# Performance work log

Hardware: AMD Instinct MI355X
Metric: run time of the kernel (lower is better)

## Reference

```python
import jax, jax.numpy as jnp
import numpy as np

B, S = 1, 2048
HID, NH, NKV, HD = 2048, 16, 4, 128
NREP = NH // NKV  # 4
WIN = 1024
ROPE_THETA = 10000.0


def rotate_half(t):
    t1, t2 = jnp.split(t, 2, axis=-1)
    return jnp.concatenate([-t2, t1], axis=-1)


def setup_inputs() -> dict:
    key = jax.random.key(0)
    ks = jax.random.split(key, 5)
    x = jax.random.normal(ks[0], (B, S, HID), dtype=jnp.float32)
    # causal sliding-window additive mask: 0 where attended, -1e9 elsewhere
    i = jnp.arange(S)
    allowed = (i[None, :] <= i[:, None]) & (i[:, None] - i[None, :] < WIN)
    attention_mask = jnp.where(allowed, 0.0, -1e9).astype(jnp.float32)[None, None]  # [1,1,S,S]
    wq = jax.random.normal(ks[1], (NH * HD, HID), dtype=jnp.float32) * 0.02
    wk = jax.random.normal(ks[2], (NKV * HD, HID), dtype=jnp.float32) * 0.02
    wv = jax.random.normal(ks[3], (NKV * HD, HID), dtype=jnp.float32) * 0.02
    wo = jax.random.normal(ks[4], (HID, NH * HD), dtype=jnp.float32) * 0.02
    return {"x": x, "attention_mask": attention_mask, "wq": wq, "wk": wk, "wv": wv, "wo": wo}


def reference(x, attention_mask, wq, wk, wv, wo):
    b, s, _ = x.shape
    q = (x @ wq.T).reshape(b, s, NH, HD)
    k = (x @ wk.T).reshape(b, s, NKV, HD)
    v = (x @ wv.T).reshape(b, s, NKV, HD)
    # rotary embeddings (HF-style rotate_half)
    inv_freq = 1.0 / (ROPE_THETA ** (jnp.arange(0, HD, 2, dtype=jnp.float32) / HD))
    freqs = jnp.arange(s, dtype=jnp.float32)[:, None] * inv_freq[None, :]  # [s, HD/2]
    emb = jnp.concatenate([freqs, freqs], axis=-1)  # [s, HD]
    cos = jnp.cos(emb)[None, :, None, :]
    sin = jnp.sin(emb)[None, :, None, :]
    q = q * cos + rotate_half(q) * sin
    k = k * cos + rotate_half(k) * sin
    # GQA: repeat kv heads
    k = jnp.repeat(k, NREP, axis=2)  # [b, s, NH, HD]
    v = jnp.repeat(v, NREP, axis=2)
    scores = jnp.einsum('bqhd,bkhd->bhqk', q, k) / jnp.sqrt(jnp.float32(HD)) + attention_mask
    probs = jax.nn.softmax(scores.astype(jnp.float32), axis=-1).astype(q.dtype)
    out = jnp.einsum('bhqk,bkhd->bqhd', probs, v).reshape(b, s, NH * HD)
    return out @ wo.T
```

## Files before the change

### kernel.cpp

```cpp
#include <hip/hip_runtime.h>


#define AS1 __attribute__((address_space(1)))
#define AS3 __attribute__((address_space(3)))

typedef short v8s __attribute__((ext_vector_type(8)));
typedef short v4s __attribute__((ext_vector_type(4)));
typedef float v4f __attribute__((ext_vector_type(4)));

__device__ __forceinline__ void gload16(const void* g, void* l) {
  __builtin_amdgcn_global_load_lds((AS1 void*)g, (AS3 void*)l, 16, 0, 0);
}

__device__ __forceinline__ short f2bf(float f) {
  union { float f; unsigned u; } v; v.f = f;
  unsigned r = (v.u + 0x7FFFu + ((v.u >> 16) & 1u)) >> 16;
  return (short)r;
}
__device__ __forceinline__ float bf2f(short h) {
  union { unsigned u; float f; } v; v.u = ((unsigned)(unsigned short)h) << 16;
  return v.f;
}
__device__ __forceinline__ bool sniff_bf16(const unsigned* mask) {
  return mask[1] == 0xCE6ECE6Eu;
}

template <bool BF> struct Raw8;
template <> struct Raw8<true>  { v8s v; };
template <> struct Raw8<false> { float4 a, b; };

template <bool BF> __device__ __forceinline__ Raw8<BF> ldraw(const void* p, size_t e);
template <> __device__ __forceinline__ Raw8<true> ldraw<true>(const void* p, size_t e) {
  Raw8<true> r; r.v = *(const v8s*)((const short*)p + e); return r;
}
template <> __device__ __forceinline__ Raw8<false> ldraw<false>(const void* p, size_t e) {
  Raw8<false> r; const float* f = (const float*)p + e;
  r.a = *(const float4*)f; r.b = *(const float4*)(f + 4); return r;
}
template <bool BF> __device__ __forceinline__ v8s cvt8(const Raw8<BF>& r);
template <> __device__ __forceinline__ v8s cvt8<true>(const Raw8<true>& r) { return r.v; }
template <> __device__ __forceinline__ v8s cvt8<false>(const Raw8<false>& r) {
  v8s o;
  o[0] = f2bf(r.a.x); o[1] = f2bf(r.a.y); o[2] = f2bf(r.a.z); o[3] = f2bf(r.a.w);
  o[4] = f2bf(r.b.x); o[5] = f2bf(r.b.y); o[6] = f2bf(r.b.z); o[7] = f2bf(r.b.w);
  return o;
}

__global__ __launch_bounds__(256) void convert_kernel(
    const void* __restrict__ X, const void* __restrict__ WQ,
    const void* __restrict__ WK, const void* __restrict__ WV,
    const void* __restrict__ WO, const unsigned* __restrict__ mask,
    short* __restrict__ Xbf, short* __restrict__ Wqkvbf, short* __restrict__ WObf)
{
  const bool bf = sniff_bf16(mask);
  size_t e = ((size_t)blockIdx.x * 256 + threadIdx.x) * 8;
  const void* src; short* dst; size_t off, doff;
  if (e < 4194304)       { src = X;  dst = Xbf;  off = e; doff = e; }
  else if (e < 10485760) {
    size_t wv = e - 4194304; dst = Wqkvbf; doff = wv;
    if (wv < 4194304)      { src = WQ; off = wv; }
    else if (wv < 5242880) { src = WK; off = wv - 4194304; }
    else                   { src = WV; off = wv - 5242880; }
  }
  else                   { src = WO; dst = WObf; off = e - 10485760; doff = off; }
  v8s v = bf ? ldraw<true>(src, off).v : cvt8<false>(ldraw<false>(src, off));
  *(v8s*)&dst[doff] = v;
}

__device__ __forceinline__ void gemm_dma_loop(
    const short* __restrict__ A, const short* __restrict__ Bt,
    int m0, int brow0, short* lA, short* lB, v4f acc[2][4])
{
  const int tid = threadIdx.x;
  const int w = tid >> 6, lane = tid & 63;
  const int quad = lane >> 4, r = lane & 15;
  const int wm = (w >> 1) * 32, wn = (w & 1) * 64;
  const int rlo = lane >> 2, c8 = (lane & 3) * 8;

  size_t ga[2]; short* la[2];
#pragma unroll
  for (int j = 0; j < 2; ++j) {
    int cA = w * 2 + j;
    int p = cA >> 2, local = cA & 3;
    ga[j] = (size_t)(m0 + local * 16 + rlo) * 2048 + p * 32 + c8;
    la[j] = lA + cA * 512;
  }
  size_t gb[4]; short* lb[4];
#pragma unroll
  for (int j = 0; j < 4; ++j) {
    int cB = w * 4 + j;
    int p = cB >> 3, local = cB & 7;
    gb[j] = (size_t)(brow0 + local * 16 + rlo) * 2048 + p * 32 + c8;
    lb[j] = lB + cB * 512;
  }

  for (int k0 = 0; k0 < 2048; k0 += 64) {
    if (k0) __syncthreads();
#pragma unroll
    for (int j = 0; j < 2; ++j) gload16(A + ga[j] + k0, la[j]);
#pragma unroll
    for (int j = 0; j < 4; ++j) gload16(Bt + gb[j] + k0, lb[j]);
    __syncthreads();
#pragma unroll
    for (int ks = 0; ks < 2; ++ks) {
      v8s a[2], b[4];
#pragma unroll
      for (int mt = 0; mt < 2; ++mt)
        a[mt] = *(const v8s*)&lA[ks * 2048 + (wm + mt * 16 + r) * 32 + quad * 8];
#pragma unroll
      for (int nt = 0; nt < 4; ++nt)
        b[nt] = *(const v8s*)&lB[ks * 4096 + (wn + nt * 16 + r) * 32 + quad * 8];
#pragma unroll
      for (int mt = 0; mt < 2; ++mt)
#pragma unroll
        for (int nt = 0; nt < 4; ++nt)
          acc[mt][nt] = __builtin_amdgcn_mfma_f32_16x16x32_bf16(a[mt], b[nt], acc[mt][nt], 0, 0, 0);
    }
  }
}

__device__ __forceinline__ void qkv_epilogue(
    v4f acc[2][4], int m0, int n0, short* Qo, short* Ko, short* VTo)
{
  const int tid = threadIdx.x;
  const int w = tid >> 6, lane = tid & 63;
  const int quad = lane >> 4, r = lane & 15;
  const int wm = (w >> 1) * 32, wn = (w & 1) * 64;
  const int rowb = m0 + wm + quad * 4;

  if (n0 < 2048) {
#pragma unroll
    for (int mt = 0; mt < 2; ++mt)
#pragma unroll
      for (int nt = 0; nt < 4; ++nt) {
        int row = rowb + mt * 16;
        int col = n0 + wn + nt * 16 + r;
#pragma unroll
        for (int i = 0; i < 4; ++i)
          Qo[(size_t)(row + i) * 2048 + col] = f2bf(acc[mt][nt][i]);
      }
  } else if (n0 < 2560) {
#pragma unroll
    for (int mt = 0; mt < 2; ++mt)
#pragma unroll
      for (int nt = 0; nt < 4; ++nt) {
        int row = rowb + mt * 16;
        int col = n0 + wn + nt * 16 + r - 2048;
#pragma unroll
        for (int i = 0; i < 4; ++i)
          Ko[(size_t)(row + i) * 512 + col] = f2bf(acc[mt][nt][i]);
      }
  } else {
#pragma unroll
    for (int mt = 0; mt < 2; ++mt)
#pragma unroll
      for (int nt = 0; nt < 4; ++nt) {
        int row = rowb + mt * 16;
        int vcol = n0 + wn + nt * 16 + r - 2560;
        v4s pk;
#pragma unroll
        for (int i = 0; i < 4; ++i) pk[i] = f2bf(acc[mt][nt][i]);
        *(v4s*)&VTo[(size_t)vcol * 2048 + row] = pk;
      }
  }
}

__global__ __launch_bounds__(256, 3) void gemm_qkv_dma(
    const short* __restrict__ Xbf, const short* __restrict__ Wqkvbf,
    short* __restrict__ Qo, short* __restrict__ Ko, short* __restrict__ VTo)
{
  __shared__ __align__(16) short lA[64 * 64];
  __shared__ __align__(16) short lB[128 * 64];
  const int m0 = blockIdx.x * 64;
  const int n0 = blockIdx.y * 128;
  v4f acc[2][4];
#pragma unroll
  for (int i = 0; i < 2; ++i)
#pragma unroll
    for (int j = 0; j < 4; ++j) acc[i][j] = v4f{0.f, 0.f, 0.f, 0.f};
  gemm_dma_loop(Xbf, Wqkvbf, m0, n0, lA, lB, acc);
  qkv_epilogue(acc, m0, n0, Qo, Ko, VTo);
}

__global__ __launch_bounds__(256, 3) void gemm_out_dma(
    const short* __restrict__ A, const short* __restrict__ WObf,
    const unsigned* __restrict__ mask, void* __restrict__ Out)
{
  __shared__ __align__(16) short lA[64 * 64];
  __shared__ __align__(16) short lB[128 * 64];
  const int m0 = blockIdx.x * 64;
  const int n0 = blockIdx.y * 128;
  v4f acc[2][4];
#pragma unroll
  for (int i = 0; i < 2; ++i)
#pragma unroll
    for (int j = 0; j < 4; ++j) acc[i][j] = v4f{0.f, 0.f, 0.f, 0.f};
  gemm_dma_loop(A, WObf, m0, n0, lA, lB, acc);

  const bool bf = sniff_bf16(mask);
  const int tid = threadIdx.x;
  const int w = tid >> 6, lane = tid & 63;
  const int quad = lane >> 4, r = lane & 15;
  const int wm = (w >> 1) * 32, wn = (w & 1) * 64;
  const int rowb = m0 + wm + quad * 4;
#pragma unroll
  for (int mt = 0; mt < 2; ++mt)
#pragma unroll
    for (int nt = 0; nt < 4; ++nt) {
      int row = rowb + mt * 16;
      int col = n0 + wn + nt * 16 + r;
#pragma unroll
      for (int i = 0; i < 4; ++i) {
        size_t idx = (size_t)(row + i) * 2048 + col;
        if (bf) ((short*)Out)[idx] = f2bf(acc[mt][nt][i]);
        else    ((float*)Out)[idx] = acc[mt][nt][i];
      }
    }
}

template <bool BFA, bool BFB>
__device__ __forceinline__ void gemm64x128_loop(
    const void* __restrict__ A, const void* __restrict__ Bt,
    int m0, int brow0, short* lA, short* lB, v4f acc[2][4])
{
  const int tid = threadIdx.x;
  const int w = tid >> 6, lane = tid & 63;
  const int quad = lane >> 4, r = lane & 15;
  const int wm = (w >> 1) * 32, wn = (w & 1) * 64;

  int uoffA[2]; size_t ea[2];
#pragma unroll
  for (int j = 0; j < 2; ++j) {
    int u = tid + 256 * j;
    int row = u >> 3, c = (u & 7) * 8;
    uoffA[j] = (c & 32) * 64 + row * 32 + (c & 31);
    ea[j] = (size_t)(m0 + row) * 2048 + c;
  }
  int uoffB[4]; size_t eb[4];
#pragma unroll
  for (int j = 0; j < 4; ++j) {
    int u = tid + 256 * j;
    int row = u >> 3, c = (u & 7) * 8;
    uoffB[j] = (c & 32) * 128 + row * 32 + (c & 31);
    eb[j] = (size_t)(brow0 + row) * 2048 + c;
  }

  for (int k0 = 0; k0 < 2048; k0 += 64) {
    Raw8<BFA> ta[2]; Raw8<BFB> tb[4];
#pragma unroll
    for (int j = 0; j < 2; ++j) ta[j] = ldraw<BFA>(A, ea[j] + k0);
#pragma unroll
    for (int j = 0; j < 4; ++j) tb[j] = ldraw<BFB>(Bt, eb[j] + k0);
    if (k0) __syncthreads();
#pragma unroll
    for (int j = 0; j < 2; ++j) *(v8s*)&lA[uoffA[j]] = cvt8<BFA>(ta[j]);
#pragma unroll
    for (int j = 0; j < 4; ++j) *(v8s*)&lB[uoffB[j]] = cvt8<BFB>(tb[j]);
    __syncthreads();
#pragma unroll
    for (int ks = 0; ks < 2; ++ks) {
      v8s a[2], b[4];
#pragma unroll
      for (int mt = 0; mt < 2; ++mt)
        a[mt] = *(const v8s*)&lA[ks * 2048 + (wm + mt * 16 + r) * 32 + quad * 8];
#pragma unroll
      for (int nt = 0; nt < 4; ++nt)
        b[nt] = *(const v8s*)&lB[ks * 4096 + (wn + nt * 16 + r) * 32 + quad * 8];
#pragma unroll
      for (int mt = 0; mt < 2; ++mt)
#pragma unroll
        for (int nt = 0; nt < 4; ++nt)
          acc[mt][nt] = __builtin_amdgcn_mfma_f32_16x16x32_bf16(a[mt], b[nt], acc[mt][nt], 0, 0, 0);
    }
  }
}

__global__ __launch_bounds__(256, 3) void gemm_qkv_fb(
    const void* __restrict__ X, const void* __restrict__ WQ,
    const void* __restrict__ WK, const void* __restrict__ WV,
    const unsigned* __restrict__ mask,
    short* __restrict__ Qo, short* __restrict__ Ko, short* __restrict__ VTo)
{
  __shared__ __align__(16) short lA[64 * 64];
  __shared__ __align__(16) short lB[128 * 64];
  const int m0 = blockIdx.x * 64;
  const int n0 = blockIdx.y * 128;
  const void* Bt; int brow0;
  if (n0 < 2048)      { Bt = WQ; brow0 = n0; }
  else if (n0 < 2560) { Bt = WK; brow0 = n0 - 2048; }
  else                { Bt = WV; brow0 = n0 - 2560; }

  v4f acc[2][4];
#pragma unroll
  for (int i = 0; i < 2; ++i)
#pragma unroll
    for (int j = 0; j < 4; ++j) acc[i][j] = v4f{0.f, 0.f, 0.f, 0.f};

  if (sniff_bf16(mask)) gemm64x128_loop<true, true>(X, Bt, m0, brow0, lA, lB, acc);
  else                  gemm64x128_loop<false, false>(X, Bt, m0, brow0, lA, lB, acc);
  qkv_epilogue(acc, m0, n0, Qo, Ko, VTo);
}

__global__ __launch_bounds__(256, 3) void gemm_out_fb(
    const short* __restrict__ A, const void* __restrict__ WO,
    const unsigned* __restrict__ mask, void* __restrict__ Out)
{
  __shared__ __align__(16) short lA[64 * 64];
  __shared__ __align__(16) short lB[128 * 64];
  const bool bf = sniff_bf16(mask);
  const int m0 = blockIdx.x * 64;
  const int n0 = blockIdx.y * 128;

  v4f acc[2][4];
#pragma unroll
  for (int i = 0; i < 2; ++i)
#pragma unroll
    for (int j = 0; j < 4; ++j) acc[i][j] = v4f{0.f, 0.f, 0.f, 0.f};

  if (bf) gemm64x128_loop<true, true>(A, WO, m0, n0, lA, lB, acc);
  else    gemm64x128_loop<true, false>(A, WO, m0, n0, lA, lB, acc);

  const int tid = threadIdx.x;
  const int w = tid >> 6, lane = tid & 63;
  const int quad = lane >> 4, r = lane & 15;
  const int wm = (w >> 1) * 32, wn = (w & 1) * 64;
  const int rowb = m0 + wm + quad * 4;
#pragma unroll
  for (int mt = 0; mt < 2; ++mt)
#pragma unroll
    for (int nt = 0; nt < 4; ++nt) {
      int row = rowb + mt * 16;
      int col = n0 + wn + nt * 16 + r;
#pragma unroll
      for (int i = 0; i < 4; ++i) {
        size_t idx = (size_t)(row + i) * 2048 + col;
        if (bf) ((short*)Out)[idx] = f2bf(acc[mt][nt][i]);
        else    ((float*)Out)[idx] = acc[mt][nt][i];
      }
    }
}

__global__ __launch_bounds__(256) void rope_kernel(short* __restrict__ Q, short* __restrict__ K)
{
  const int t = blockIdx.x * 256 + threadIdx.x;
  const float L2T = 13.287712379549449f / 64.0f;
  int s, d; short* p; float scale;
  if (t < 2097152) {
    s = t >> 10; int rem = t & 1023; int h = rem >> 6; d = rem & 63;
    p = Q + (size_t)s * 2048 + h * 128 + d;
    scale = 0.08838834764831845f;
  } else {
    int u = t - 2097152;
    s = u >> 8; int rem = u & 255; int h = rem >> 6; d = rem & 63;
    p = K + (size_t)s * 512 + h * 128 + d;
    scale = 1.0f;
  }
  float inv = exp2f(-(float)d * L2T);
  float ang = (float)s * inv;
  float cs = cosf(ang), sn = sinf(ang);
  float x1 = bf2f(p[0]), x2 = bf2f(p[64]);
  p[0]  = f2bf((x1 * cs - x2 * sn) * scale);
  p[64] = f2bf((x2 * cs + x1 * sn) * scale);
}

__global__ __launch_bounds__(256, 1) void attn_kernel(
    const short* __restrict__ Q, const short* __restrict__ Kb,
    const short* __restrict__ VT, short* __restrict__ Ao)
{
  __shared__ __align__(16) short lK[64 * 128];
  __shared__ __align__(16) short lV[128 * 64];
  __shared__ __align__(16) short lP[4][16 * 72];

  const int bx = blockIdx.x;
  const int h = bx >> 5, qb = bx & 31;
  const int hk = h >> 2;
  const int q0 = qb * 64;
  const int tid = threadIdx.x, w = tid >> 6, lane = tid & 63;
  const int quad = lane >> 4, r = lane & 15;
  const int wq0 = q0 + w * 16;
  short* lPw = lP[w];

  v8s qa[4];
#pragma unroll
  for (int ks = 0; ks < 4; ++ks)
    qa[ks] = *(const v8s*)(Q + (size_t)(wq0 + r) * 2048 + h * 128 + ks * 32 + quad * 8);

  v4f Oa[8];
#pragma unroll
  for (int dt = 0; dt < 8; ++dt) Oa[dt] = v4f{0.f, 0.f, 0.f, 0.f};
  const float NEG = -3.0e38f;
  float m_i[4], l_i[4];
#pragma unroll
  for (int i = 0; i < 4; ++i) { m_i[i] = NEG; l_i[i] = 0.f; }

  const int t0 = (q0 >= 1024) ? ((q0 - 1023) >> 6) : 0;
  const int t1 = qb;

  for (int t = t0; t <= t1; ++t) {
    const int key0 = t << 6;
    v8s tK[4], tV[4];
#pragma unroll
    for (int u = 0; u < 4; ++u) {
      int lin = (w * 4 + u) * 64 + lane;
      int krow = lin >> 4, kcc = lin & 15;
      tK[u] = *(const v8s*)(Kb + (size_t)(key0 + krow) * 512 + hk * 128 + ((kcc ^ krow) & 15) * 8);
      int vrow = lin >> 3, vcc = lin & 7;
      tV[u] = *(const v8s*)(VT + (size_t)(hk * 128 + vrow) * 2048 + key0 + ((vcc ^ vrow) & 7) * 8);
    }
    if (t > t0) __syncthreads();
#pragma unroll
    for (int u = 0; u < 4; ++u) {
      int lin = (w * 4 + u) * 64 + lane;
      *(v8s*)&lK[lin * 8] = tK[u];
      *(v8s*)&lV[lin * 8] = tV[u];
    }
    __syncthreads();

    v4f s4[4];
#pragma unroll
    for (int nt = 0; nt < 4; ++nt) s4[nt] = v4f{0.f, 0.f, 0.f, 0.f};
#pragma unroll
    for (int ks = 0; ks < 4; ++ks)
#pragma unroll
      for (int nt = 0; nt < 4; ++nt) {
        v8s bk = *(const v8s*)&lK[(nt * 16 + r) * 128 + (((ks * 4 + quad) ^ r) & 15) * 8];
        s4[nt] = __builtin_amdgcn_mfma_f32_16x16x32_bf16(qa[ks], bk, s4[nt], 0, 0, 0);
      }

    float rowmax[4] = {NEG, NEG, NEG, NEG};
#pragma unroll
    for (int nt = 0; nt < 4; ++nt) {
      int key = key0 + nt * 16 + r;
#pragma unroll
      for (int i = 0; i < 4; ++i) {
        int q = wq0 + quad * 4 + i;
        bool ok = (key <= q) && (q - key < 1024);
        if (ok) rowmax[i] = fmaxf(rowmax[i], s4[nt][i]);
      }
    }
#pragma unroll
    for (int i = 0; i < 4; ++i)
#pragma unroll
      for (int off = 1; off < 16; off <<= 1)
        rowmax[i] = fmaxf(rowmax[i], __shfl_xor(rowmax[i], off, 64));
    float alpha[4], rsum[4] = {0.f, 0.f, 0.f, 0.f};
#pragma unroll
    for (int i = 0; i < 4; ++i) {
      float mn = fmaxf(m_i[i], rowmax[i]);
      alpha[i] = __expf(m_i[i] - mn);
      m_i[i] = mn;
    }
#pragma unroll
    for (int nt = 0; nt < 4; ++nt) {
      int key = key0 + nt * 16 + r;
#pragma unroll
      for (int i = 0; i < 4; ++i) {
        int q = wq0 + quad * 4 + i;
        bool ok = (key <= q) && (q - key < 1024);
        float p = ok ? __expf(s4[nt][i] - m_i[i]) : 0.0f;
        rsum[i] += p;
        lPw[(quad * 4 + i) * 72 + nt * 16 + r] = f2bf(p);
      }
    }
#pragma unroll
    for (int i = 0; i < 4; ++i) {
#pragma unroll
      for (int off = 1; off < 16; off <<= 1)
        rsum[i] += __shfl_xor(rsum[i], off, 64);
      l_i[i] = l_i[i] * alpha[i] + rsum[i];
    }
#pragma unroll
    for (int dt = 0; dt < 8; ++dt)
#pragma unroll
      for (int i = 0; i < 4; ++i) Oa[dt][i] *= alpha[i];

#pragma unroll
    for (int ks2 = 0; ks2 < 2; ++ks2) {
      v8s ap = *(const v8s*)&lPw[r * 72 + ks2 * 32 + quad * 8];
#pragma unroll
      for (int dt = 0; dt < 8; ++dt) {
        v8s bv = *(const v8s*)&lV[(dt * 16 + r) * 64 + (((ks2 * 4 + quad) ^ r) & 7) * 8];
        Oa[dt] = __builtin_amdgcn_mfma_f32_16x16x32_bf16(ap, bv, Oa[dt], 0, 0, 0);
      }
    }
  }

  float invl[4];
#pragma unroll
  for (int i = 0; i < 4; ++i) invl[i] = (l_i[i] > 0.f) ? 1.0f / l_i[i] : 0.f;
#pragma unroll
  for (int dt = 0; dt < 8; ++dt)
#pragma unroll
    for (int i = 0; i < 4; ++i) {
      int q = wq0 + quad * 4 + i;
      Ao[(size_t)q * 2048 + h * 128 + dt * 16 + r] = f2bf(Oa[dt][i] * invl[i]);
    }
}

extern "C" void kernel_launch(void* const* d_in, const int* in_sizes, int n_in,
                              void* d_out, int out_size, void* d_ws, size_t ws_size,
                              hipStream_t stream) {
  const void*     x    = d_in[0];
  const unsigned* mask = (const unsigned*)d_in[1];
  const void*     wq   = d_in[2];
  const void*     wk   = d_in[3];
  const void*     wv   = d_in[4];
  const void*     wo   = d_in[5];

  short* Q  = (short*)d_out;
  short* Kb = (short*)d_ws;
  short* VT = Kb + (size_t)1048576;
  short* Ao = VT + (size_t)1048576;

  const size_t NEED = 41943040ull;
  if (ws_size >= NEED) {
    short* Xbf    = Ao + (size_t)4194304;
    short* Wqkvbf = Xbf + (size_t)4194304;
    short* WObf   = Wqkvbf + (size_t)6291456;
    convert_kernel<<<7168, 256, 0, stream>>>(x, wq, wk, wv, wo, mask, Xbf, Wqkvbf, WObf);
    gemm_qkv_dma<<<dim3(32, 24), 256, 0, stream>>>(Xbf, Wqkvbf, Q, Kb, VT);
    rope_kernel<<<10240, 256, 0, stream>>>(Q, Kb);
    attn_kernel<<<512, 256, 0, stream>>>(Q, Kb, VT, Ao);
    gemm_out_dma<<<dim3(32, 16), 256, 0, stream>>>(Ao, WObf, mask, d_out);
  } else {
    gemm_qkv_fb<<<dim3(32, 24), 256, 0, stream>>>(x, wq, wk, wv, mask, Q, Kb, VT);
    rope_kernel<<<10240, 256, 0, stream>>>(Q, Kb);
    attn_kernel<<<512, 256, 0, stream>>>(Q, Kb, VT, Ao);
    gemm_out_fb<<<dim3(32, 16), 256, 0, stream>>>(Ao, wo, mask, d_out);
  }
}
```

Before: 229.9 us.

## Fuse RoPE and softmax scale into QKV GEMM epilogue, skip masks on full tiles

Removes the separate rope kernel. A new column mapping lets each wave hold both halves (d and d+64) of a head in its accumulators, so RoPE and the Q scale (folded with log2e) are applied in the QKV GEMM epilogue. Attention now uses exp2f on the prescaled scores, skips the per-element mask checks on tiles that are fully inside the window, and reorders the block index so heads of the same query block run adjacently. This saves one kernel launch and a full read-modify-write of Q and K. In exchange, the GEMM epilogue gets heavier trig work and the column layout of every GEMM changes.

```diff
diff --git a/kernel.cpp b/kernel.cpp
--- a/kernel.cpp
+++ b/kernel.cpp
@@ -24,6 +24,13 @@
 __device__ __forceinline__ bool sniff_bf16(const unsigned* mask) {
   return mask[1] == 0xCE6ECE6Eu;
 }
+
+__device__ __forceinline__ int colmap(int w, int nt, int r) {
+  return (w & 1) * 32 + (nt & 1) * 16 + (nt >> 1) * 64 + r;
+}
+
+#define ROPE_L2T (13.287712379549449f / 64.0f)
+#define Q_SCALE  (1.4426950408889634f * 0.08838834764831845f)
 
 template <bool BF> struct Raw8;
 template <> struct Raw8<true>  { v8s v; };
@@ -74,7 +81,7 @@
   const int tid = threadIdx.x;
   const int w = tid >> 6, lane = tid & 63;
   const int quad = lane >> 4, r = lane & 15;
-  const int wm = (w >> 1) * 32, wn = (w & 1) * 64;
+  const int wm = (w >> 1) * 32;
   const int rlo = lane >> 2, c8 = (lane & 3) * 8;
 
   size_t ga[2]; short* la[2];
@@ -109,7 +116,7 @@
         a[mt] = *(const v8s*)&lA[ks * 2048 + (wm + mt * 16 + r) * 32 + quad * 8];
 #pragma unroll
       for (int nt = 0; nt < 4; ++nt)
-        b[nt] = *(const v8s*)&lB[ks * 4096 + (wn + nt * 16 + r) * 32 + quad * 8];
+        b[nt] = *(const v8s*)&lB[ks * 4096 + colmap(w, nt, r) * 32 + quad * 8];
 #pragma unroll
       for (int mt = 0; mt < 2; ++mt)
 #pragma unroll
@@ -125,38 +132,38 @@
   const int tid = threadIdx.x;
   const int w = tid >> 6, lane = tid & 63;
   const int quad = lane >> 4, r = lane & 15;
-  const int wm = (w >> 1) * 32, wn = (w & 1) * 64;
+  const int wm = (w >> 1) * 32;
   const int rowb = m0 + wm + quad * 4;
 
-  if (n0 < 2048) {
+  if (n0 < 2560) {
+    const bool isQ = (n0 < 2048);
+    short* dst = isQ ? Qo : Ko;
+    const int ld = isQ ? 2048 : 512;
+    const int base = isQ ? n0 : (n0 - 2048);
+    const float sc = isQ ? Q_SCALE : 1.0f;
+#pragma unroll
+    for (int nt = 0; nt < 2; ++nt) {
+      int d = (w & 1) * 32 + nt * 16 + r;
+      float inv = exp2f(-(float)d * ROPE_L2T);
+#pragma unroll
+      for (int mt = 0; mt < 2; ++mt)
+#pragma unroll
+        for (int i = 0; i < 4; ++i) {
+          int row = rowb + mt * 16 + i;
+          float ang = (float)row * inv;
+          float cs = cosf(ang), sn = sinf(ang);
+          float x1 = acc[mt][nt][i], x2 = acc[mt][nt + 2][i];
+          dst[(size_t)row * ld + base + d]      = f2bf((x1 * cs - x2 * sn) * sc);
+          dst[(size_t)row * ld + base + d + 64] = f2bf((x2 * cs + x1 * sn) * sc);
+        }
+    }
+  } else {
 #pragma unroll
     for (int mt = 0; mt < 2; ++mt)
 #pragma unroll
       for (int nt = 0; nt < 4; ++nt) {
         int row = rowb + mt * 16;
-        int col = n0 + wn + nt * 16 + r;
-#pragma unroll
-        for (int i = 0; i < 4; ++i)
-          Qo[(size_t)(row + i) * 2048 + col] = f2bf(acc[mt][nt][i]);
-      }
-  } else if (n0 < 2560) {
-#pragma unroll
-    for (int mt = 0; mt < 2; ++mt)
-#pragma unroll
-      for (int nt = 0; nt < 4; ++nt) {
-        int row = rowb + mt * 16;
-        int col = n0 + wn + nt * 16 + r - 2048;
-#pragma unroll
-        for (int i = 0; i < 4; ++i)
-          Ko[(size_t)(row + i) * 512 + col] = f2bf(acc[mt][nt][i]);
-      }
-  } else {
-#pragma unroll
-    for (int mt = 0; mt < 2; ++mt)
-#pragma unroll
-      for (int nt = 0; nt < 4; ++nt) {
-        int row = rowb + mt * 16;
-        int vcol = n0 + wn + nt * 16 + r - 2560;
+        int vcol = n0 - 2560 + colmap(w, nt, r);
         v4s pk;
 #pragma unroll
         for (int i = 0; i < 4; ++i) pk[i] = f2bf(acc[mt][nt][i]);
@@ -201,14 +208,14 @@
   const int tid = threadIdx.x;
   const int w = tid >> 6, lane = tid & 63;
   const int quad = lane >> 4, r = lane & 15;
-  const int wm = (w >> 1) * 32, wn = (w & 1) * 64;
+  const int wm = (w >> 1) * 32;
   const int rowb = m0 + wm + quad * 4;
 #pragma unroll
   for (int mt = 0; mt < 2; ++mt)
 #pragma unroll
     for (int nt = 0; nt < 4; ++nt) {
       int row = rowb + mt * 16;
-      int col = n0 + wn + nt * 16 + r;
+      int col = n0 + colmap(w, nt, r);
 #pragma unroll
       for (int i = 0; i < 4; ++i) {
         size_t idx = (size_t)(row + i) * 2048 + col;
@@ -226,7 +233,7 @@
   const int tid = threadIdx.x;
   const int w = tid >> 6, lane = tid & 63;
   const int quad = lane >> 4, r = lane & 15;
-  const int wm = (w >> 1) * 32, wn = (w & 1) * 64;
+  const int wm = (w >> 1) * 32;
 
   int uoffA[2]; size_t ea[2];
 #pragma unroll
@@ -265,7 +272,7 @@
         a[mt] = *(const v8s*)&lA[ks * 2048 + (wm + mt * 16 + r) * 32 + quad * 8];
 #pragma unroll
       for (int nt = 0; nt < 4; ++nt)
-        b[nt] = *(const v8s*)&lB[ks * 4096 + (wn + nt * 16 + r) * 32 + quad * 8];
+        b[nt] = *(const v8s*)&lB[ks * 4096 + colmap(w, nt, r) * 32 + quad * 8];
 #pragma unroll
       for (int mt = 0; mt < 2; ++mt)
 #pragma unroll
@@ -323,14 +330,14 @@
   const int tid = threadIdx.x;
   const int w = tid >> 6, lane = tid & 63;
   const int quad = lane >> 4, r = lane & 15;
-  const int wm = (w >> 1) * 32, wn = (w & 1) * 64;
+  const int wm = (w >> 1) * 32;
   const int rowb = m0 + wm + quad * 4;
 #pragma unroll
   for (int mt = 0; mt < 2; ++mt)
 #pragma unroll
     for (int nt = 0; nt < 4; ++nt) {
       int row = rowb + mt * 16;
-      int col = n0 + wn + nt * 16 + r;
+      int col = n0 + colmap(w, nt, r);
 #pragma unroll
       for (int i = 0; i < 4; ++i) {
         size_t idx = (size_t)(row + i) * 2048 + col;
@@ -340,29 +347,6 @@
     }
 }
 
-__global__ __launch_bounds__(256) void rope_kernel(short* __restrict__ Q, short* __restrict__ K)
-{
-  const int t = blockIdx.x * 256 + threadIdx.x;
-  const float L2T = 13.287712379549449f / 64.0f;
-  int s, d; short* p; float scale;
-  if (t < 2097152) {
-    s = t >> 10; int rem = t & 1023; int h = rem >> 6; d = rem & 63;
-    p = Q + (size_t)s * 2048 + h * 128 + d;
-    scale = 0.08838834764831845f;
-  } else {
-    int u = t - 2097152;
-    s = u >> 8; int rem = u & 255; int h = rem >> 6; d = rem & 63;
-    p = K + (size_t)s * 512 + h * 128 + d;
-    scale = 1.0f;
-  }
-  float inv = exp2f(-(float)d * L2T);
-  float ang = (float)s * inv;
-  float cs = cosf(ang), sn = sinf(ang);
-  float x1 = bf2f(p[0]), x2 = bf2f(p[64]);
-  p[0]  = f2bf((x1 * cs - x2 * sn) * scale);
-  p[64] = f2bf((x2 * cs + x1 * sn) * scale);
-}
-
 __global__ __launch_bounds__(256, 1) void attn_kernel(
     const short* __restrict__ Q, const short* __restrict__ Kb,
     const short* __restrict__ VT, short* __restrict__ Ao)
@@ -372,7 +356,7 @@
   __shared__ __align__(16) short lP[4][16 * 72];
 
   const int bx = blockIdx.x;
-  const int h = bx >> 5, qb = bx & 31;
+  const int qb = bx >> 4, h = bx & 15;
   const int hk = h >> 2;
   const int q0 = qb * 64;
   const int tid = threadIdx.x, w = tid >> 6, lane = tid & 63;
@@ -427,15 +411,24 @@
         s4[nt] = __builtin_amdgcn_mfma_f32_16x16x32_bf16(qa[ks], bk, s4[nt], 0, 0, 0);
       }
 
+    const bool full = (key0 + 63 <= wq0) && (wq0 + 15 - key0 < 1024);
+
     float rowmax[4] = {NEG, NEG, NEG, NEG};
-#pragma unroll
-    for (int nt = 0; nt < 4; ++nt) {
-      int key = key0 + nt * 16 + r;
-#pragma unroll
-      for (int i = 0; i < 4; ++i) {
-        int q = wq0 + quad * 4 + i;
-        bool ok = (key <= q) && (q - key < 1024);
-        if (ok) rowmax[i] = fmaxf(rowmax[i], s4[nt][i]);
+    if (full) {
+#pragma unroll
+      for (int nt = 0; nt < 4; ++nt)
+#pragma unroll
+        for (int i = 0; i < 4; ++i) rowmax[i] = fmaxf(rowmax[i], s4[nt][i]);
+    } else {
+#pragma unroll
+      for (int nt = 0; nt < 4; ++nt) {
+        int key = key0 + nt * 16 + r;
+#pragma unroll
+        for (int i = 0; i < 4; ++i) {
+          int q = wq0 + quad * 4 + i;
+          bool ok = (key <= q) && (q - key < 1024);
+          if (ok) rowmax[i] = fmaxf(rowmax[i], s4[nt][i]);
+        }
       }
     }
 #pragma unroll
@@ -447,19 +440,30 @@
 #pragma unroll
     for (int i = 0; i < 4; ++i) {
       float mn = fmaxf(m_i[i], rowmax[i]);
-      alpha[i] = __expf(m_i[i] - mn);
+      alpha[i] = exp2f(m_i[i] - mn);
       m_i[i] = mn;
     }
-#pragma unroll
-    for (int nt = 0; nt < 4; ++nt) {
-      int key = key0 + nt * 16 + r;
-#pragma unroll
-      for (int i = 0; i < 4; ++i) {
-        int q = wq0 + quad * 4 + i;
-        bool ok = (key <= q) && (q - key < 1024);
-        float p = ok ? __expf(s4[nt][i] - m_i[i]) : 0.0f;
-        rsum[i] += p;
-        lPw[(quad * 4 + i) * 72 + nt * 16 + r] = f2bf(p);
+    if (full) {
+#pragma unroll
+      for (int nt = 0; nt < 4; ++nt)
+#pragma unroll
+        for (int i = 0; i < 4; ++i) {
+          float p = exp2f(s4[nt][i] - m_i[i]);
+          rsum[i] += p;
+          lPw[(quad * 4 + i) * 72 + nt * 16 + r] = f2bf(p);
+        }
+    } else {
+#pragma unroll
+      for (int nt = 0; nt < 4; ++nt) {
+        int key = key0 + nt * 16 + r;
+#pragma unroll
+        for (int i = 0; i < 4; ++i) {
+          int q = wq0 + quad * 4 + i;
+          bool ok = (key <= q) && (q - key < 1024);
+          float p = ok ? exp2f(s4[nt][i] - m_i[i]) : 0.0f;
+          rsum[i] += p;
+          lPw[(quad * 4 + i) * 72 + nt * 16 + r] = f2bf(p);
+        }
       }
     }
 #pragma unroll
@@ -519,12 +523,10 @@
     short* WObf   = Wqkvbf + (size_t)6291456;
     convert_kernel<<<7168, 256, 0, stream>>>(x, wq, wk, wv, wo, mask, Xbf, Wqkvbf, WObf);
     gemm_qkv_dma<<<dim3(32, 24), 256, 0, stream>>>(Xbf, Wqkvbf, Q, Kb, VT);
-    rope_kernel<<<10240, 256, 0, stream>>>(Q, Kb);
     attn_kernel<<<512, 256, 0, stream>>>(Q, Kb, VT, Ao);
     gemm_out_dma<<<dim3(32, 16), 256, 0, stream>>>(Ao, WObf, mask, d_out);
   } else {
     gemm_qkv_fb<<<dim3(32, 24), 256, 0, stream>>>(x, wq, wk, wv, mask, Q, Kb, VT);
-    rope_kernel<<<10240, 256, 0, stream>>>(Q, Kb);
     attn_kernel<<<512, 256, 0, stream>>>(Q, Kb, VT, Ao);
     gemm_out_fb<<<dim3(32, 16), 256, 0, stream>>>(Ao, wo, mask, d_out);
   }
```

Result: no change. 227.4 us (-1.1%).
